# Performance work log

Measured on AMD Instinct MI355X. Metric: run time of the kernel, lower is better.

## Reference

```python
import jax, jax.numpy as jnp
import numpy as np

WS = 6          # window size
NUM_HEADS = 6
HEAD_DIM = 32   # dim=192 / 6 heads
SCALE = HEAD_DIM ** -0.5


def _rel_pos_index(ws):
    # Faithful to the torch buffer construction (torch.meshgrid default 'ij').
    coords = np.stack(np.meshgrid(np.arange(ws), np.arange(ws), np.arange(ws), indexing='ij'))  # [3,ws,ws,ws]
    flat = coords.reshape(3, -1)                       # [3, ws^3]
    rel = flat[:, :, None] - flat[:, None, :]          # [3, N, N]
    rel = rel.transpose(1, 2, 0).astype(np.int64)      # [N, N, 3]
    rel += ws - 1
    rel[..., 0] *= 3 * ws - 1
    rel[..., 1] *= 2 * ws - 1
    return rel.sum(-1)                                 # [N, N]

REL_INDEX = jnp.asarray(_rel_pos_index(WS))            # [216, 216] int


def setup_inputs() -> dict:
    key = jax.random.key(0)
    k1, k2, k3, k4 = jax.random.split(key, 4)
    B, N, C = 1024, WS ** 3, NUM_HEADS * HEAD_DIM
    return {
        "x": jax.random.normal(k1, (B, N, C), dtype=jnp.float32),
        "qkv_w": jax.random.normal(k2, (3 * C, C), dtype=jnp.float32) * 0.02,
        "proj_w": jax.random.normal(k3, (C, C), dtype=jnp.float32) * 0.02,
        "proj_b": jnp.zeros((C,), dtype=jnp.float32),
        "bias_table": jax.random.normal(k4, ((2 * WS - 1) ** 3, NUM_HEADS), dtype=jnp.float32) * 0.02,
    }


def reference(x, qkv_w, proj_w, proj_b, bias_table):
    B, N, C = x.shape
    H, D = NUM_HEADS, HEAD_DIM
    qkv = jnp.einsum('bnc,fc->bnf', x, qkv_w)              # [B,N,3C]
    qkv = qkv.reshape(B, N, 3, H, D).transpose(2, 0, 3, 1, 4)  # [3,B,H,N,D]
    q, k, v = qkv[0], qkv[1], qkv[2]
    attn = jnp.einsum('bhnd,bhmd->bhnm', q * SCALE, k)     # [B,H,N,N]
    bias = bias_table[REL_INDEX]                           # [N,N,H]
    attn = attn + bias.transpose(2, 0, 1)[None]            # add [1,H,N,N]
    attn = jax.nn.softmax(attn, axis=-1)
    out = jnp.einsum('bhnm,bhmd->bhnd', attn, v)           # [B,H,N,D]
    out = out.transpose(0, 2, 1, 3).reshape(B, N, C)
    return jnp.einsum('bnc,oc->bno', out, proj_w) + proj_b
```

## Files before the change

### kernel.cpp

```cpp
#include <hip/hip_runtime.h>
#include <cstdint>
#include <cstddef>


typedef __attribute__((ext_vector_type(8))) short short8;
typedef __attribute__((ext_vector_type(4))) float f32x4;
typedef unsigned short u16;
typedef unsigned int   u32;

#define SCALE_F 0.17677669529663687f

#define XS_OFF   0
#define QS_OFF   89600
#define KS_OFF   107520
#define VT_OFF   125440
#define PCH_OFF  140288
#define ATTN_LDS 158208

#define PROJ_AS_OFF  0
#define PROJ_PW_OFF  86400
#define PROJ_LDS     163200

__device__ __forceinline__ u16 f2bf(float f) {
  union { float f; u32 u; } v; v.f = f;
  return (u16)((v.u + 0x7fffu + ((v.u >> 16) & 1u)) >> 16);
}

__device__ __forceinline__ f32x4 mfma16(short8 a, short8 b, f32x4 c) {
  return __builtin_amdgcn_mfma_f32_16x16x32_bf16(a, b, c, 0, 0, 0);
}

__global__ void prep_kernel(const float* __restrict__ qkv_w,
                            const float* __restrict__ proj_w,
                            const float* __restrict__ bias_table,
                            u16* __restrict__ wb,
                            u16* __restrict__ pwb,
                            u16* __restrict__ biasp) {
  const int tid = blockIdx.x * blockDim.x + threadIdx.x;
  const int stride = gridDim.x * blockDim.x;
  for (int i = tid; i < 576 * 192; i += stride) wb[i] = f2bf(qkv_w[i]);
  for (int i = tid; i < 192 * 192; i += stride) pwb[i] = f2bf(proj_w[i]);
  for (int i = tid; i < 6 * 7 * 16 * 224 * 2; i += stride) {
    const int t = i & 1;
    int j = i >> 1;
    const int n = j % 224; j /= 224;
    const int l = j & 15;  j >>= 4;
    const int c = j % 7;
    const int h = j / 7;
    const int m = c * 32 + t * 16 + l;
    u16 val;
    if (n >= 216)      val = 0;
    else if (m >= 216) val = 0xFF80;
    else {
      const int di = n / 36 - m / 36;
      const int dj = (n / 6) % 6 - (m / 6) % 6;
      const int dk = n % 6 - m % 6;
      const int idx = (di + 5) * 17 + (dj + 5) * 11 + (dk + 5);
      val = f2bf(bias_table[idx * 6 + h]);
    }
    biasp[i] = val;
  }
}

__global__ __launch_bounds__(1024, 4)
void attn_kernel(const float* __restrict__ x, const u16* __restrict__ wb,
                 const u16* __restrict__ biasp, float* __restrict__ outbuf) {
  extern __shared__ char smem[];
  u16* xs  = (u16*)(smem + XS_OFF);
  u16* qs  = (u16*)(smem + QS_OFF);
  u16* ks  = (u16*)(smem + KS_OFF);
  u16* vT  = (u16*)(smem + VT_OFF);
  u16* pch = (u16*)(smem + PCH_OFF);

  const int b = blockIdx.x;
  const int tid = threadIdx.x;
  const int wave = tid >> 6;
  const int lane = tid & 63;
  const int quad = lane >> 4;
  const int lcol = lane & 15;

  {
    const float4* xg4 = (const float4*)(x + (size_t)b * 41472);
    for (int i = tid; i < 216 * 48; i += 1024) {
      const int row = i / 48, c4 = i % 48;
      const float4 v = xg4[row * 48 + c4];
      union { u16 s[4]; unsigned long long u; } pk;
      pk.s[0] = f2bf(v.x); pk.s[1] = f2bf(v.y);
      pk.s[2] = f2bf(v.z); pk.s[3] = f2bf(v.w);
      *(unsigned long long*)(xs + row * 200 + c4 * 4) = pk.u;
    }
    for (int i = tid; i < 8 * 40; i += 1024) { qs[216 * 40 + i] = 0; ks[216 * 40 + i] = 0; }
    for (int i = tid; i < 32 * 8; i += 1024) {
      const int d = i >> 3, jj = i & 7;
      vT[d * 232 + 209 + 2 * jj] = 0;
    }
  }
  __syncthreads();

  u16* attnb = (u16*)(outbuf + (size_t)b * 41472);

  for (int h = 0; h < 6; ++h) {
    for (int u = wave; u < 14; u += 16) {
      f32x4 acc[6] = {};
#pragma unroll
      for (int kk = 0; kk < 6; ++kk) {
        const short8 a = *(const short8*)(xs + (u * 16 + lcol) * 200 + kk * 32 + quad * 8);
#pragma unroll
        for (int j = 0; j < 6; ++j) {
          const int fbase = (j >> 1) * 192 + h * 32 + (j & 1) * 16;
          const short8 bf = *(const short8*)(wb + (fbase + lcol) * 192 + kk * 32 + quad * 8);
          acc[j] = mfma16(a, bf, acc[j]);
        }
      }
      const int nb = u * 16 + quad * 4;
#pragma unroll
      for (int r = 0; r < 4; ++r) {
        const int n = nb + r;
        if (n < 216) {
          *(u32*)(qs + n * 40 + 2 * lcol) =
              (u32)f2bf(acc[0][r]) | ((u32)f2bf(acc[1][r]) << 16);
          *(u32*)(ks + n * 40 + 2 * lcol) =
              (u32)f2bf(acc[2][r]) | ((u32)f2bf(acc[3][r]) << 16);
          const int pm = (n & ~31) | (2 * (n & 15)) | ((n >> 4) & 1);
          vT[lcol * 232 + pm]        = f2bf(acc[4][r]);
          vT[(16 + lcol) * 232 + pm] = f2bf(acc[5][r]);
        }
      }
    }
    __syncthreads();

    if (wave < 14) {
      const int s = wave;
      u16* pw_ = pch + wave * 640;

      uint4 bias_q[7];
#pragma unroll
      for (int c = 0; c < 7; ++c)
        bias_q[c] = *(const uint4*)(biasp + ((size_t)((h * 7 + c) * 16 + lcol)) * 448
                                    + (s * 16 + quad * 4) * 2);
      const short8 qa = *(const short8*)(qs + (s * 16 + lcol) * 40 + quad * 8);

      u32 pP[7][4];
      f32x4 rsum = {};
#pragma unroll
      for (int c = 0; c < 7; ++c) {
        const short8 kb0 = *(const short8*)(ks + (c * 32 + lcol) * 40 + quad * 8);
        const short8 kb1 = *(const short8*)(ks + (c * 32 + 16 + lcol) * 40 + quad * 8);
        const f32x4 z = {};
        const f32x4 s0 = mfma16(qa, kb0, z);
        const f32x4 s1 = mfma16(qa, kb1, z);
        const u32* bw = (const u32*)&bias_q[c];
#pragma unroll
        for (int r = 0; r < 4; ++r) {
          union { u32 u; float f; } b0, b1;
          b0.u = bw[r] << 16;
          b1.u = bw[r] & 0xFFFF0000u;
          const float p0 = __expf(__builtin_fmaf(s0[r], SCALE_F, b0.f));
          const float p1 = __expf(__builtin_fmaf(s1[r], SCALE_F, b1.f));
          rsum[r] += p0 + p1;
          pP[c][r] = (u32)f2bf(p0) | ((u32)f2bf(p1) << 16);
        }
      }

      f32x4 o0 = {}, o1 = {};
#pragma unroll
      for (int c = 0; c < 7; ++c) {
#pragma unroll
        for (int r = 0; r < 4; ++r)
          *(u32*)(pw_ + (quad * 4 + r) * 40 + 2 * lcol) = pP[c][r];
        __builtin_amdgcn_s_waitcnt(0);
        const short8 pa  = *(const short8*)(pw_ + lcol * 40 + quad * 8);
        const short8 vb0 = *(const short8*)(vT + lcol * 232 + c * 32 + quad * 8);
        const short8 vb1 = *(const short8*)(vT + (16 + lcol) * 232 + c * 32 + quad * 8);
        o0 = mfma16(pa, vb0, o0);
        o1 = mfma16(pa, vb1, o1);
      }

      f32x4 inv;
#pragma unroll
      for (int r = 0; r < 4; ++r) {
        float ssum = rsum[r];
        ssum += __shfl_xor(ssum, 1, 16);
        ssum += __shfl_xor(ssum, 2, 16);
        ssum += __shfl_xor(ssum, 4, 16);
        ssum += __shfl_xor(ssum, 8, 16);
        inv[r] = 1.0f / ssum;
      }
#pragma unroll
      for (int r = 0; r < 4; ++r) {
        const int n = s * 16 + quad * 4 + r;
        if (n < 216) {
          attnb[n * 192 + h * 32 + lcol]      = f2bf(o0[r] * inv[r]);
          attnb[n * 192 + h * 32 + 16 + lcol] = f2bf(o1[r] * inv[r]);
        }
      }
    }
    __syncthreads();
  }
}

__global__ __launch_bounds__(1024, 4)
void proj_kernel(const u16* __restrict__ pwb, const float* __restrict__ proj_b,
                 float* __restrict__ outbuf) {
  extern __shared__ char smem[];
  u16* as  = (u16*)(smem + PROJ_AS_OFF);
  u16* pws = (u16*)(smem + PROJ_PW_OFF);
  const int b = blockIdx.x, tid = threadIdx.x;
  const int wave = tid >> 6, lane = tid & 63, quad = lane >> 4, lcol = lane & 15;
  float* myout = outbuf + (size_t)b * 41472;
  const u16* attnb = (const u16*)myout;

  for (int i = tid; i < 216 * 24; i += 1024) {
    const int row = i / 24, c8 = i % 24;
    *(short8*)(as + row * 200 + c8 * 8) = *(const short8*)(attnb + row * 192 + c8 * 8);
  }
  for (int i = tid; i < 192 * 24; i += 1024) {
    const int row = i / 24, c8 = i % 24;
    *(short8*)(pws + row * 200 + c8 * 8) = *(const short8*)(pwb + row * 192 + c8 * 8);
  }
  __syncthreads();

  for (int u = wave; u < 14; u += 16) {
    const int arow = u * 16 + lcol;
    const bool ok = arow < 216;
    short8 a[6];
#pragma unroll
    for (int kk = 0; kk < 6; ++kk) {
      const short8 z = {};
      a[kk] = ok ? *(const short8*)(as + arow * 200 + kk * 32 + quad * 8) : z;
    }
    for (int nt = 0; nt < 12; ++nt) {
      f32x4 acc = {};
#pragma unroll
      for (int kk = 0; kk < 6; ++kk) {
        const short8 bf = *(const short8*)(pws + (nt * 16 + lcol) * 200 + kk * 32 + quad * 8);
        acc = mfma16(a[kk], bf, acc);
      }
      const float pbv = proj_b[nt * 16 + lcol];
      const int nb = u * 16 + quad * 4;
#pragma unroll
      for (int r = 0; r < 4; ++r) {
        const int n = nb + r;
        if (n < 216) myout[n * 192 + nt * 16 + lcol] = acc[r] + pbv;
      }
    }
  }
}

extern "C" void kernel_launch(void* const* d_in, const int* in_sizes, int n_in,
                              void* d_out, int out_size, void* d_ws, size_t ws_size,
                              hipStream_t stream) {
  (void)in_sizes; (void)n_in; (void)out_size; (void)ws_size;
  const float* x          = (const float*)d_in[0];
  const float* qkv_w      = (const float*)d_in[1];
  const float* proj_w     = (const float*)d_in[2];
  const float* proj_b     = (const float*)d_in[3];
  const float* bias_table = (const float*)d_in[4];
  float* out = (float*)d_out;

  u16* wb    = (u16*)d_ws;
  u16* pwb   = (u16*)((char*)d_ws + 221184);
  u16* biasp = (u16*)((char*)d_ws + 294912);

  (void)hipFuncSetAttribute((const void*)attn_kernel,
                            hipFuncAttributeMaxDynamicSharedMemorySize, ATTN_LDS);
  (void)hipFuncSetAttribute((const void*)proj_kernel,
                            hipFuncAttributeMaxDynamicSharedMemorySize, PROJ_LDS);

  prep_kernel<<<dim3(512), dim3(256), 0, stream>>>(qkv_w, proj_w, bias_table, wb, pwb, biasp);
  attn_kernel<<<dim3(1024), dim3(1024), ATTN_LDS, stream>>>(x, wb, biasp, out);
  proj_kernel<<<dim3(1024), dim3(1024), PROJ_LDS, stream>>>(pwb, proj_b, out);
}
```

Before: 814.4 us.

## Pre-convert x to bf16 in prep kernel and drop LDS staging of activations

The fp32-to-bf16 conversion of x moves into the prep kernel, which writes bf16 x into the upper half of each batch's output slot. The attention kernel then reads A fragments straight from global memory instead of staging x in LDS, and the projection kernel loads its A fragments directly into registers. LDS use drops from about 158KB to 69KB (attn) and 163KB to 77KB (proj), and launch bounds rise to allow more resident blocks. The cost is an extra global round trip for x in bf16, plus repeated global reads of x across the six heads.

```diff
diff --git a/kernel.cpp b/kernel.cpp
--- a/kernel.cpp
+++ b/kernel.cpp
@@ -10,16 +10,13 @@
 
 #define SCALE_F 0.17677669529663687f
 
-#define XS_OFF   0
-#define QS_OFF   89600
-#define KS_OFF   107520
-#define VT_OFF   125440
-#define PCH_OFF  140288
-#define ATTN_LDS 158208
-
-#define PROJ_AS_OFF  0
-#define PROJ_PW_OFF  86400
-#define PROJ_LDS     163200
+#define QS_OFF   0
+#define KS_OFF   17920
+#define VT_OFF   35840
+#define PCH_OFF  50688
+#define ATTN_LDS 68608
+
+#define PROJ_LDS 76800
 
 __device__ __forceinline__ u16 f2bf(float f) {
   union { float f; u32 u; } v; v.f = f;
@@ -30,14 +27,25 @@
   return __builtin_amdgcn_mfma_f32_16x16x32_bf16(a, b, c, 0, 0, 0);
 }
 
-__global__ void prep_kernel(const float* __restrict__ qkv_w,
+__global__ void prep_kernel(const float* __restrict__ x,
+                            const float* __restrict__ qkv_w,
                             const float* __restrict__ proj_w,
                             const float* __restrict__ bias_table,
                             u16* __restrict__ wb,
                             u16* __restrict__ pwb,
-                            u16* __restrict__ biasp) {
+                            u16* __restrict__ biasp,
+                            float* outbuf) {
   const int tid = blockIdx.x * blockDim.x + threadIdx.x;
   const int stride = gridDim.x * blockDim.x;
+  const float4* x4 = (const float4*)x;
+  for (int i = tid; i < 1024 * 10368; i += stride) {
+    const int b = i / 10368, r = i % 10368;
+    const float4 v = x4[i];
+    union { u16 s[4]; unsigned long long u; } pk;
+    pk.s[0] = f2bf(v.x); pk.s[1] = f2bf(v.y);
+    pk.s[2] = f2bf(v.z); pk.s[3] = f2bf(v.w);
+    *(unsigned long long*)((u16*)(outbuf + (size_t)b * 41472) + 41472 + r * 4) = pk.u;
+  }
   for (int i = tid; i < 576 * 192; i += stride) wb[i] = f2bf(qkv_w[i]);
   for (int i = tid; i < 192 * 192; i += stride) pwb[i] = f2bf(proj_w[i]);
   for (int i = tid; i < 6 * 7 * 16 * 224 * 2; i += stride) {
@@ -62,11 +70,10 @@
   }
 }
 
-__global__ __launch_bounds__(1024, 4)
-void attn_kernel(const float* __restrict__ x, const u16* __restrict__ wb,
-                 const u16* __restrict__ biasp, float* __restrict__ outbuf) {
+__global__ __launch_bounds__(1024, 8)
+void attn_kernel(const u16* __restrict__ wb, const u16* __restrict__ biasp,
+                 float* outbuf) {
   extern __shared__ char smem[];
-  u16* xs  = (u16*)(smem + XS_OFF);
   u16* qs  = (u16*)(smem + QS_OFF);
   u16* ks  = (u16*)(smem + KS_OFF);
   u16* vT  = (u16*)(smem + VT_OFF);
@@ -79,32 +86,24 @@
   const int quad = lane >> 4;
   const int lcol = lane & 15;
 
-  {
-    const float4* xg4 = (const float4*)(x + (size_t)b * 41472);
-    for (int i = tid; i < 216 * 48; i += 1024) {
-      const int row = i / 48, c4 = i % 48;
-      const float4 v = xg4[row * 48 + c4];
-      union { u16 s[4]; unsigned long long u; } pk;
-      pk.s[0] = f2bf(v.x); pk.s[1] = f2bf(v.y);
-      pk.s[2] = f2bf(v.z); pk.s[3] = f2bf(v.w);
-      *(unsigned long long*)(xs + row * 200 + c4 * 4) = pk.u;
-    }
-    for (int i = tid; i < 8 * 40; i += 1024) { qs[216 * 40 + i] = 0; ks[216 * 40 + i] = 0; }
-    for (int i = tid; i < 32 * 8; i += 1024) {
-      const int d = i >> 3, jj = i & 7;
-      vT[d * 232 + 209 + 2 * jj] = 0;
-    }
+  const u16* xb   = (const u16*)(outbuf + (size_t)b * 41472) + 41472;
+  u16*       attnb = (u16*)(outbuf + (size_t)b * 41472);
+
+  for (int i = tid; i < 8 * 40; i += 1024) { qs[216 * 40 + i] = 0; ks[216 * 40 + i] = 0; }
+  for (int i = tid; i < 32 * 8; i += 1024) {
+    const int d = i >> 3, jj = i & 7;
+    vT[d * 232 + 209 + 2 * jj] = 0;
   }
   __syncthreads();
-
-  u16* attnb = (u16*)(outbuf + (size_t)b * 41472);
 
   for (int h = 0; h < 6; ++h) {
     for (int u = wave; u < 14; u += 16) {
       f32x4 acc[6] = {};
+      const int ar0 = u * 16 + lcol;
+      const int ar  = ar0 < 216 ? ar0 : 215;
 #pragma unroll
       for (int kk = 0; kk < 6; ++kk) {
-        const short8 a = *(const short8*)(xs + (u * 16 + lcol) * 200 + kk * 32 + quad * 8);
+        const short8 a = *(const short8*)(xb + ar * 192 + kk * 32 + quad * 8);
 #pragma unroll
         for (int j = 0; j < 6; ++j) {
           const int fbase = (j >> 1) * 192 + h * 32 + (j & 1) * 16;
@@ -199,36 +198,34 @@
   }
 }
 
-__global__ __launch_bounds__(1024, 4)
+__global__ __launch_bounds__(1024, 8)
 void proj_kernel(const u16* __restrict__ pwb, const float* __restrict__ proj_b,
-                 float* __restrict__ outbuf) {
+                 float* outbuf) {
   extern __shared__ char smem[];
-  u16* as  = (u16*)(smem + PROJ_AS_OFF);
-  u16* pws = (u16*)(smem + PROJ_PW_OFF);
+  u16* pws = (u16*)smem;
   const int b = blockIdx.x, tid = threadIdx.x;
   const int wave = tid >> 6, lane = tid & 63, quad = lane >> 4, lcol = lane & 15;
   float* myout = outbuf + (size_t)b * 41472;
   const u16* attnb = (const u16*)myout;
 
-  for (int i = tid; i < 216 * 24; i += 1024) {
-    const int row = i / 24, c8 = i % 24;
-    *(short8*)(as + row * 200 + c8 * 8) = *(const short8*)(attnb + row * 192 + c8 * 8);
-  }
   for (int i = tid; i < 192 * 24; i += 1024) {
     const int row = i / 24, c8 = i % 24;
     *(short8*)(pws + row * 200 + c8 * 8) = *(const short8*)(pwb + row * 192 + c8 * 8);
   }
+
+  short8 a[6] = {};
+  const bool active = wave < 14;
+  if (active) {
+    const int arow = wave * 16 + lcol;
+    if (arow < 216) {
+#pragma unroll
+      for (int kk = 0; kk < 6; ++kk)
+        a[kk] = *(const short8*)(attnb + arow * 192 + kk * 32 + quad * 8);
+    }
+  }
   __syncthreads();
 
-  for (int u = wave; u < 14; u += 16) {
-    const int arow = u * 16 + lcol;
-    const bool ok = arow < 216;
-    short8 a[6];
-#pragma unroll
-    for (int kk = 0; kk < 6; ++kk) {
-      const short8 z = {};
-      a[kk] = ok ? *(const short8*)(as + arow * 200 + kk * 32 + quad * 8) : z;
-    }
+  if (active) {
     for (int nt = 0; nt < 12; ++nt) {
       f32x4 acc = {};
 #pragma unroll
@@ -237,7 +234,7 @@
         acc = mfma16(a[kk], bf, acc);
       }
       const float pbv = proj_b[nt * 16 + lcol];
-      const int nb = u * 16 + quad * 4;
+      const int nb = wave * 16 + quad * 4;
 #pragma unroll
       for (int r = 0; r < 4; ++r) {
         const int n = nb + r;
@@ -267,7 +264,8 @@
   (void)hipFuncSetAttribute((const void*)proj_kernel,
                             hipFuncAttributeMaxDynamicSharedMemorySize, PROJ_LDS);
 
-  prep_kernel<<<dim3(512), dim3(256), 0, stream>>>(qkv_w, proj_w, bias_table, wb, pwb, biasp);
-  attn_kernel<<<dim3(1024), dim3(1024), ATTN_LDS, stream>>>(x, wb, biasp, out);
+  prep_kernel<<<dim3(1024), dim3(256), 0, stream>>>(x, qkv_w, proj_w, bias_table,
+                                                    wb, pwb, biasp, out);
+  attn_kernel<<<dim3(1024), dim3(1024), ATTN_LDS, stream>>>(wb, biasp, out);
   proj_kernel<<<dim3(1024), dim3(1024), PROJ_LDS, stream>>>(pwb, proj_b, out);
 }
```

New measurement: 812.7 us. No clear change (-0.2%).
